# Kernel optimization log

Measured on AMD Instinct MI355X. Metric: run time of the kernel, lower is better.

## Reference

```python
import jax, jax.numpy as jnp
import numpy as np
from jax import lax

SPIKE_RATE = 100.0
TIME_STEPS = 100
ADAPT_FACTOR = 0.95
REFRACTORY = 2.0
N_NEURONS = 256


def setup_inputs() -> dict:
    key = jax.random.key(0)
    x = jax.random.normal(jax.random.fold_in(key, 1), (32, 64), dtype=jnp.float32)
    centers = jnp.linspace(-1.0, 1.0, N_NEURONS).astype(jnp.float32)
    widths = jnp.full((N_NEURONS,), 0.2, dtype=jnp.float32)
    adaptation_state = jnp.ones((N_NEURONS,), dtype=jnp.float32)
    refractory_state = jnp.zeros((N_NEURONS,), dtype=jnp.float32)
    return {
        "x": x,
        "centers": centers,
        "widths": widths,
        "adaptation_state": adaptation_state,
        "refractory_state": refractory_state,
        "seed": 0,
    }


def reference(x, centers, widths, adaptation_state, refractory_state, seed):
    # x: [B, F]; centers/widths/states: [N]
    # Gaussian tuning-curve response: [B, F, N]
    d = x[:, :, None] - centers[None, None, :]
    response = jnp.exp(-(d * d) / (2.0 * widths * widths))
    # adaptation applied once with the initial buffer state (as in torch source)
    response = response * adaptation_state[None, None, :]
    spike_prob = response * (SPIKE_RATE / 1000.0)

    base_key = jax.random.key(seed)

    def step(carry, t):
        ref, adapt = carry  # each [N]
        k = jax.random.fold_in(base_key, t)
        r = jax.random.uniform(k, spike_prob.shape, dtype=spike_prob.dtype)
        can_spike = (ref == 0).astype(spike_prob.dtype)  # [N]
        spike_t = (r < spike_prob).astype(spike_prob.dtype) * can_spike[None, None, :]
        ref = jnp.maximum(ref - 1.0, 0.0)
        occurred = spike_t.sum(axis=(0, 1)) > 0  # [N]
        ref = ref + occurred.astype(ref.dtype) * REFRACTORY
        adapt = adapt * jnp.where(occurred, ADAPT_FACTOR, 1.0)
        return (ref, adapt), spike_t

    (_, _), spikes = lax.scan(step, (refractory_state, adaptation_state),
                              jnp.arange(TIME_STEPS))
    # spikes: [T, B, F, N] -> [B, F, N, T] to match torch.stack(..., dim=-1)
    return jnp.moveaxis(spikes, 0, -1)
```

## Files before the change

### kernel.cpp

```cpp
#include <hip/hip_runtime.h>
#include <stdint.h>

typedef unsigned long long u64;
typedef unsigned int u32;

#define T_STEPS 100
#define NNEUR 256
#define NBF 2048
#define NELEM (NBF * NNEUR)

__device__ __forceinline__ void tf2x32(u32 k0, u32 k1, u32& x0, u32& x1) {
  u32 k2 = k0 ^ k1 ^ 0x1BD11BDAu;
  x0 += k0; x1 += k1;
#define TFR(r) { x0 += x1; x1 = (x1 << (r)) | (x1 >> (32 - (r))); x1 ^= x0; }
  TFR(13) TFR(15) TFR(26) TFR(6)
  x0 += k1; x1 += k2 + 1u;
  TFR(17) TFR(29) TFR(16) TFR(24)
  x0 += k2; x1 += k0 + 2u;
  TFR(13) TFR(15) TFR(26) TFR(6)
  x0 += k0; x1 += k1 + 3u;
  TFR(17) TFR(29) TFR(16) TFR(24)
  x0 += k1; x1 += k2 + 4u;
  TFR(13) TFR(15) TFR(26) TFR(6)
  x0 += k2; x1 += k0 + 5u;
#undef TFR
}

__device__ __forceinline__ u32 rotl32(u32 x, int r) {
  return __builtin_amdgcn_alignbit(x, x, 32 - r);
}

__global__ void __launch_bounds__(256) kern_p(
    const float* __restrict__ x, const float* __restrict__ c,
    const float* __restrict__ w, const float* __restrict__ a,
    u32* __restrict__ thr9) {
  int idx = blockIdx.x * 256 + threadIdx.x;
  int n = idx & 255, bf = idx >> 8;
  float d = x[bf] - c[n];
  float denom = (2.0f * w[n]) * w[n];
  float q = -(d * d) / denom;
  float e = (float)exp((double)q);
  float p = (e * a[n]) * 0.1f;
  thr9[idx] = ((u32)ceilf(p * 8388608.0f)) << 9;
}

__global__ void __launch_bounds__(256, 4) kern_bits2(
    const u32* __restrict__ thr9,
    const int* __restrict__ seedp,
    u32* __restrict__ cmp32,
    u32* __restrict__ occ32) {
  const int t = blockIdx.x;
  const int g = blockIdx.y;
  const int tid = threadIdx.x;
  const int oct = tid & 7;
  const int bfl = tid >> 3;
  const int bf = g * 32 + bfl;
  const u32 seed = (u32)seedp[0];

  u32 K0 = 0u, K1 = (u32)t;
  tf2x32(0u, seed, K0, K1);
  const u32 K2 = K0 ^ K1 ^ 0x1BD11BDAu;
  const u32 I10 = K1;
  const u32 I11 = K2 + 1u;
  const u32 I20 = K2;
  const u32 I21 = K0 + 2u;
  const u32 I30 = K0;
  const u32 I31 = K1 + 3u;
  const u32 I40 = K1;
  const u32 I41 = K2 + 4u;
  const u32 I50 = K2;
  const u32 I51 = K0 + 5u;

  const u32 base_i = (u32)(bf * 256 + oct * 32);

  u32 th[32];
  const uint4* tp = (const uint4*)(thr9 + base_i);
#pragma unroll
  for (int q = 0; q < 8; ++q) {
    uint4 v = tp[q];
    th[4*q] = v.x; th[4*q+1] = v.y; th[4*q+2] = v.z; th[4*q+3] = v.w;
  }

  const u32 x1base = base_i + K1;
  const u32 x0base = x1base + K0;
  u32 word = 0u;
#pragma unroll
  for (int k = 31; k >= 0; --k) {
    u32 x1 = x1base + (u32)k;
    u32 x0 = x0base + (u32)k;
    x1 = rotl32(x1, 13); x1 ^= x0;
#define QR(r) { x0 += x1; x1 = rotl32(x1, r); x1 ^= x0; }
    QR(15) QR(26) QR(6)
    x0 += I10; x1 += I11;
    QR(17) QR(29) QR(16) QR(24)
    x0 += I20; x1 += I21;
    QR(13) QR(15) QR(26) QR(6)
    x0 += I30; x1 += I31;
    QR(17) QR(29) QR(16) QR(24)
    x0 += I40; x1 += I41;
    QR(13) QR(15) QR(26) QR(6)
    x0 += I50; x1 += I51;
#undef QR
    word = (word << 1) | ((x0 ^ x1) < th[k] ? 1u : 0u);
  }

  cmp32[((u32)bf * T_STEPS + (u32)t) * 8 + oct] = word;

  u32 o = word;
  o |= (u32)__shfl_xor((int)o, 8, 64);
  o |= (u32)__shfl_xor((int)o, 16, 64);
  o |= (u32)__shfl_xor((int)o, 32, 64);
  if ((tid & 63) < 8) atomicOr(&occ32[t * 8 + oct], o);
}

__global__ void __launch_bounds__(256) kern_out2(
    const u32* __restrict__ cmp32,
    const u32* __restrict__ occ32,
    const float* __restrict__ ref0,
    float* __restrict__ out) {
  __shared__ u32 s_occ[T_STEPS * 8];
  __shared__ u32 s_can[T_STEPS * 8];
  __shared__ u32 s[T_STEPS * 8];
  const int bf = blockIdx.x;
  const int tid = threadIdx.x;

  for (int l = tid; l < T_STEPS * 8; l += 256) s_occ[l] = occ32[l];
  __syncthreads();

  {
    const int n = tid, lane = n & 63, v = n >> 6;
    float ref = ref0[n];
    for (int t = 0; t < T_STEPS; ++t) {
      bool can = (ref == 0.0f);
      u64 cm = __ballot(can);
      if (lane == 0) {
        s_can[t * 8 + v * 2]     = (u32)cm;
        s_can[t * 8 + v * 2 + 1] = (u32)(cm >> 32);
      }
      bool occb = (s_occ[t * 8 + (n >> 5)] >> (n & 31)) & 1u;
      bool occurred = can && occb;
      ref = fmaxf(ref - 1.0f, 0.0f) + (occurred ? 2.0f : 0.0f);
    }
  }
  __syncthreads();

  for (int l = tid; l < T_STEPS * 8; l += 256) {
    int t = l >> 3, ww = l & 7;
    s[l] = cmp32[((u64)bf * T_STEPS + (u64)t) * 8 + ww] & s_can[l];
  }
  __syncthreads();

  float4* outv = (float4*)(out + (u64)bf * (NNEUR * T_STEPS));
#pragma unroll
  for (int kk = 0; kk < 25; ++kk) {
    int q = tid + 256 * kk;
    int e = q * 4;
    float4 val;
    float* vp = (float*)&val;
#pragma unroll
    for (int j = 0; j < 4; ++j) {
      int ee = e + j;
      int n = ee / 100;
      int t = ee - n * 100;
      vp[j] = (float)((s[t * 8 + (n >> 5)] >> (n & 31)) & 1u);
    }
    outv[q] = val;
  }
}

__global__ void __launch_bounds__(256) kern_bits_fb(
    const float* __restrict__ x, const float* __restrict__ c,
    const float* __restrict__ w, const float* __restrict__ a,
    const int* __restrict__ seedp,
    float* __restrict__ outf,
    u64* __restrict__ occ64) {
  const int t = blockIdx.x;
  const int chunk = blockIdx.y;
  const int lane = threadIdx.x & 63;
  const int v = threadIdx.x >> 6;
  const int n = v * 64 + lane;
  const u32 seed = (u32)seedp[0];
  u32 kt0 = 0u, kt1 = (u32)t;
  tf2x32(0u, seed, kt0, kt1);
  float cn = c[n], wn = w[n], an = a[n];
  bool occ = false;
  for (int j = 0; j < 64; ++j) {
    int bf = chunk * 64 + j;
    u32 i = (u32)(bf * 256 + n);
    u32 b0 = 0u, b1 = i;
    tf2x32(kt0, kt1, b0, b1);
    u32 bits = b0 ^ b1;
    float r = __uint_as_float((bits >> 9) | 0x3F800000u) - 1.0f;
    float d = x[bf] - cn;
    float denom = (2.0f * wn) * wn;
    float q = -(d * d) / denom;
    float pv = ((float)exp((double)q) * an) * 0.1f;
    bool cm = r < pv;
    occ |= cm;
    outf[(u64)bf * (NNEUR * T_STEPS) + (u64)n * T_STEPS + t] = cm ? 1.0f : 0.0f;
  }
  u64 om = __ballot(occ);
  if (lane == 0) atomicOr(&occ64[t * 4 + v], om);
}

__global__ void __launch_bounds__(256) kern_rec(
    const float* __restrict__ ref0,
    const u64* __restrict__ occ64,
    u64* __restrict__ can64) {
  int n = threadIdx.x;
  int lane = n & 63, v = n >> 6;
  float ref = ref0[n];
  for (int t = 0; t < T_STEPS; ++t) {
    bool can = (ref == 0.0f);
    u64 cm = __ballot(can);
    if (lane == 0) can64[t * 4 + v] = cm;
    bool occb = (occ64[t * 4 + v] >> lane) & 1ull;
    bool occurred = can && occb;
    ref = fmaxf(ref - 1.0f, 0.0f) + (occurred ? 2.0f : 0.0f);
  }
}

__global__ void __launch_bounds__(256) kern_mask(
    const u32* __restrict__ can32, float* __restrict__ out) {
  u64 q = (u64)blockIdx.x * 256 + threadIdx.x;
  float4* ov = (float4*)out;
  float4 vx = ov[q];
  u32 local = (u32)((q * 4) % (NNEUR * T_STEPS));
  float* vp = (float*)&vx;
#pragma unroll
  for (int j = 0; j < 4; ++j) {
    u32 le = local + j;
    u32 n = le / 100;
    u32 t = le - n * 100;
    u32 bit = (can32[t * 8 + (n >> 5)] >> (n & 31)) & 1u;
    vp[j] = bit ? vp[j] : 0.0f;
  }
  ov[q] = vx;
}

extern "C" void kernel_launch(void* const* d_in, const int* in_sizes, int n_in,
                              void* d_out, int out_size, void* d_ws, size_t ws_size,
                              hipStream_t stream) {
  const float* x  = (const float*)d_in[0];
  const float* c  = (const float*)d_in[1];
  const float* w  = (const float*)d_in[2];
  const float* a  = (const float*)d_in[3];
  const float* r0 = (const float*)d_in[4];
  const int* seed = (const int*)d_in[5];
  float* out = (float*)d_out;

  const size_t P_BYTES   = (size_t)NELEM * 4;
  const size_t CMP_BYTES = (size_t)NBF * T_STEPS * 4 * 8;
  const size_t OCC_BYTES = (size_t)T_STEPS * 4 * 8;
  const bool full = ws_size >= P_BYTES + CMP_BYTES + 2 * OCC_BYTES;

  uint8_t* wsb = (uint8_t*)d_ws;

  if (full) {
    u32* thr   = (u32*)wsb;
    u32* cmp   = (u32*)(wsb + P_BYTES);
    u32* occ   = (u32*)(wsb + P_BYTES + CMP_BYTES);
    hipMemsetAsync(occ, 0, OCC_BYTES, stream);
    kern_p<<<NELEM / 256, 256, 0, stream>>>(x, c, w, a, thr);
    kern_bits2<<<dim3(T_STEPS, 64), 256, 0, stream>>>(thr, seed, cmp, occ);
    kern_out2<<<NBF, 256, 0, stream>>>(cmp, occ, r0, out);
  } else {
    u64* occ = (u64*)wsb;
    u64* can = (u64*)(wsb + OCC_BYTES);
    hipMemsetAsync(occ, 0, OCC_BYTES, stream);
    kern_bits_fb<<<dim3(T_STEPS, 32), 256, 0, stream>>>(x, c, w, a, seed, out, occ);
    kern_rec<<<1, 256, 0, stream>>>(r0, occ, can);
    kern_mask<<<(out_size / 4) / 256, 256, 0, stream>>>((const u32*)can, out);
  }
}
```

Before: 364.1 us.

## Fold occ memset into threshold kernel, batch timesteps per block, nontemporal output stores

Zeroing of the occurrence buffer moves into the threshold kernel, which removes the separate memset launch. The bits kernel now handles four timesteps per block, so each threshold load is reused across those steps and the launch uses fewer blocks. The output kernel prefetches its compare words as uint4 before the recurrence and reuses shared memory for occ, and it writes output with nontemporal vector stores to avoid polluting the cache. Having fewer blocks in the bits kernel may lower parallelism.

New measurement: 379.5 us. 1.04x slower.

```diff
diff --git a/kernel.cpp b/kernel.cpp
--- a/kernel.cpp
+++ b/kernel.cpp
@@ -3,11 +3,13 @@
 
 typedef unsigned long long u64;
 typedef unsigned int u32;
+typedef float f32x4 __attribute__((ext_vector_type(4)));
 
 #define T_STEPS 100
 #define NNEUR 256
 #define NBF 2048
 #define NELEM (NBF * NNEUR)
+#define T_PER_BLK 4
 
 __device__ __forceinline__ void tf2x32(u32 k0, u32 k1, u32& x0, u32& x1) {
   u32 k2 = k0 ^ k1 ^ 0x1BD11BDAu;
@@ -33,7 +35,7 @@
 __global__ void __launch_bounds__(256) kern_p(
     const float* __restrict__ x, const float* __restrict__ c,
     const float* __restrict__ w, const float* __restrict__ a,
-    u32* __restrict__ thr9) {
+    u32* __restrict__ thr9, u32* __restrict__ occ32) {
   int idx = blockIdx.x * 256 + threadIdx.x;
   int n = idx & 255, bf = idx >> 8;
   float d = x[bf] - c[n];
@@ -42,6 +44,9 @@
   float e = (float)exp((double)q);
   float p = (e * a[n]) * 0.1f;
   thr9[idx] = ((u32)ceilf(p * 8388608.0f)) << 9;
+  if (blockIdx.x == 0 && threadIdx.x < 200) {
+    ((uint4*)occ32)[threadIdx.x] = make_uint4(0u, 0u, 0u, 0u);
+  }
 }
 
 __global__ void __launch_bounds__(256, 4) kern_bits2(
@@ -49,28 +54,13 @@
     const int* __restrict__ seedp,
     u32* __restrict__ cmp32,
     u32* __restrict__ occ32) {
-  const int t = blockIdx.x;
+  const int t0 = blockIdx.x * T_PER_BLK;
   const int g = blockIdx.y;
   const int tid = threadIdx.x;
   const int oct = tid & 7;
   const int bfl = tid >> 3;
   const int bf = g * 32 + bfl;
   const u32 seed = (u32)seedp[0];
-
-  u32 K0 = 0u, K1 = (u32)t;
-  tf2x32(0u, seed, K0, K1);
-  const u32 K2 = K0 ^ K1 ^ 0x1BD11BDAu;
-  const u32 I10 = K1;
-  const u32 I11 = K2 + 1u;
-  const u32 I20 = K2;
-  const u32 I21 = K0 + 2u;
-  const u32 I30 = K0;
-  const u32 I31 = K1 + 3u;
-  const u32 I40 = K1;
-  const u32 I41 = K2 + 4u;
-  const u32 I50 = K2;
-  const u32 I51 = K0 + 5u;
-
   const u32 base_i = (u32)(bf * 256 + oct * 32);
 
   u32 th[32];
@@ -81,36 +71,56 @@
     th[4*q] = v.x; th[4*q+1] = v.y; th[4*q+2] = v.z; th[4*q+3] = v.w;
   }
 
-  const u32 x1base = base_i + K1;
-  const u32 x0base = x1base + K0;
-  u32 word = 0u;
-#pragma unroll
-  for (int k = 31; k >= 0; --k) {
-    u32 x1 = x1base + (u32)k;
-    u32 x0 = x0base + (u32)k;
-    x1 = rotl32(x1, 13); x1 ^= x0;
+  u32* cmp_base = cmp32 + (u32)bf * (T_STEPS * 8) + oct;
+
+#pragma unroll 1
+  for (int tt = 0; tt < T_PER_BLK; ++tt) {
+    const int t = t0 + tt;
+    u32 K0 = 0u, K1 = (u32)t;
+    tf2x32(0u, seed, K0, K1);
+    const u32 K2 = K0 ^ K1 ^ 0x1BD11BDAu;
+    const u32 I10 = K1;
+    const u32 I11 = K2 + 1u;
+    const u32 I20 = K2;
+    const u32 I21 = K0 + 2u;
+    const u32 I30 = K0;
+    const u32 I31 = K1 + 3u;
+    const u32 I40 = K1;
+    const u32 I41 = K2 + 4u;
+    const u32 I50 = K2;
+    const u32 I51 = K0 + 5u;
+
+    const u32 x1base = base_i + K1;
+    const u32 x0base = x1base + K0;
+    u32 word = 0u;
+#pragma unroll
+    for (int k = 31; k >= 0; --k) {
+      u32 x1 = x1base + (u32)k;
+      u32 x0 = x0base + (u32)k;
+      x1 = rotl32(x1, 13); x1 ^= x0;
 #define QR(r) { x0 += x1; x1 = rotl32(x1, r); x1 ^= x0; }
-    QR(15) QR(26) QR(6)
-    x0 += I10; x1 += I11;
-    QR(17) QR(29) QR(16) QR(24)
-    x0 += I20; x1 += I21;
-    QR(13) QR(15) QR(26) QR(6)
-    x0 += I30; x1 += I31;
-    QR(17) QR(29) QR(16) QR(24)
-    x0 += I40; x1 += I41;
-    QR(13) QR(15) QR(26) QR(6)
-    x0 += I50; x1 += I51;
+      QR(15) QR(26) QR(6)
+      x0 += I10; x1 += I11;
+      QR(17) QR(29) QR(16) QR(24)
+      x0 += I20; x1 += I21;
+      QR(13) QR(15) QR(26) QR(6)
+      x0 += I30; x1 += I31;
+      QR(17) QR(29) QR(16) QR(24)
+      x0 += I40; x1 += I41;
+      QR(13) QR(15) QR(26) QR(6)
+      x0 += I50; x1 += I51;
 #undef QR
-    word = (word << 1) | ((x0 ^ x1) < th[k] ? 1u : 0u);
-  }
-
-  cmp32[((u32)bf * T_STEPS + (u32)t) * 8 + oct] = word;
-
-  u32 o = word;
-  o |= (u32)__shfl_xor((int)o, 8, 64);
-  o |= (u32)__shfl_xor((int)o, 16, 64);
-  o |= (u32)__shfl_xor((int)o, 32, 64);
-  if ((tid & 63) < 8) atomicOr(&occ32[t * 8 + oct], o);
+      word = (word << 1) | ((x0 ^ x1) < th[k] ? 1u : 0u);
+    }
+
+    cmp_base[t * 8] = word;
+
+    u32 o = word;
+    o |= (u32)__shfl_xor((int)o, 8, 64);
+    o |= (u32)__shfl_xor((int)o, 16, 64);
+    o |= (u32)__shfl_xor((int)o, 32, 64);
+    if ((tid & 63) < 8) atomicOr(&occ32[t * 8 + oct], o);
+  }
 }
 
 __global__ void __launch_bounds__(256) kern_out2(
@@ -118,13 +128,15 @@
     const u32* __restrict__ occ32,
     const float* __restrict__ ref0,
     float* __restrict__ out) {
-  __shared__ u32 s_occ[T_STEPS * 8];
   __shared__ u32 s_can[T_STEPS * 8];
   __shared__ u32 s[T_STEPS * 8];
   const int bf = blockIdx.x;
   const int tid = threadIdx.x;
 
-  for (int l = tid; l < T_STEPS * 8; l += 256) s_occ[l] = occ32[l];
+  uint4 myc = make_uint4(0u, 0u, 0u, 0u);
+  if (tid < 200) myc = ((const uint4*)(cmp32 + (u64)bf * (T_STEPS * 8)))[tid];
+
+  if (tid < 200) ((uint4*)s)[tid] = ((const uint4*)occ32)[tid];
   __syncthreads();
 
   {
@@ -137,34 +149,36 @@
         s_can[t * 8 + v * 2]     = (u32)cm;
         s_can[t * 8 + v * 2 + 1] = (u32)(cm >> 32);
       }
-      bool occb = (s_occ[t * 8 + (n >> 5)] >> (n & 31)) & 1u;
+      bool occb = (s[t * 8 + (n >> 5)] >> (n & 31)) & 1u;
       bool occurred = can && occb;
       ref = fmaxf(ref - 1.0f, 0.0f) + (occurred ? 2.0f : 0.0f);
     }
   }
   __syncthreads();
 
-  for (int l = tid; l < T_STEPS * 8; l += 256) {
-    int t = l >> 3, ww = l & 7;
-    s[l] = cmp32[((u64)bf * T_STEPS + (u64)t) * 8 + ww] & s_can[l];
+  if (tid < 200) {
+    uint4 cn = ((const uint4*)s_can)[tid];
+    uint4 r;
+    r.x = myc.x & cn.x; r.y = myc.y & cn.y;
+    r.z = myc.z & cn.z; r.w = myc.w & cn.w;
+    ((uint4*)s)[tid] = r;
   }
   __syncthreads();
 
-  float4* outv = (float4*)(out + (u64)bf * (NNEUR * T_STEPS));
+  f32x4* outv = (f32x4*)(out + (u64)bf * (NNEUR * T_STEPS));
 #pragma unroll
   for (int kk = 0; kk < 25; ++kk) {
     int q = tid + 256 * kk;
     int e = q * 4;
-    float4 val;
-    float* vp = (float*)&val;
+    f32x4 val;
 #pragma unroll
     for (int j = 0; j < 4; ++j) {
       int ee = e + j;
       int n = ee / 100;
       int t = ee - n * 100;
-      vp[j] = (float)((s[t * 8 + (n >> 5)] >> (n & 31)) & 1u);
+      val[j] = (float)((s[t * 8 + (n >> 5)] >> (n & 31)) & 1u);
     }
-    outv[q] = val;
+    __builtin_nontemporal_store(val, &outv[q]);
   }
 }
 
@@ -260,9 +274,8 @@
     u32* thr   = (u32*)wsb;
     u32* cmp   = (u32*)(wsb + P_BYTES);
     u32* occ   = (u32*)(wsb + P_BYTES + CMP_BYTES);
-    hipMemsetAsync(occ, 0, OCC_BYTES, stream);
-    kern_p<<<NELEM / 256, 256, 0, stream>>>(x, c, w, a, thr);
-    kern_bits2<<<dim3(T_STEPS, 64), 256, 0, stream>>>(thr, seed, cmp, occ);
+    kern_p<<<NELEM / 256, 256, 0, stream>>>(x, c, w, a, thr, occ);
+    kern_bits2<<<dim3(T_STEPS / T_PER_BLK, 64), 256, 0, stream>>>(thr, seed, cmp, occ);
     kern_out2<<<NBF, 256, 0, stream>>>(cmp, occ, r0, out);
   } else {
     u64* occ = (u64*)wsb;
```
